# Kernel optimization log

Measured on AMD Instinct MI355X. Metric: run time of the kernel, lower is better.

## Reference

```python
import jax, jax.numpy as jnp
import numpy as np

N_NODES = 100000
N_EDGES = 1600000
EMBED_DIM = 64


def setup_inputs() -> dict:
    key = jax.random.key(0)
    k1, k2, k3, k4 = jax.random.split(key, 4)
    ego_embeddings = jax.random.normal(k1, (N_NODES, EMBED_DIM), dtype=jnp.float32)
    adj_values = jax.random.uniform(k2, (N_EDGES,), dtype=jnp.float32)
    adj_rows = jax.random.randint(k3, (N_EDGES,), 0, N_NODES, dtype=jnp.int32)
    adj_cols = jax.random.randint(k4, (N_EDGES,), 0, N_NODES, dtype=jnp.int32)
    return {
        "ego_embeddings": ego_embeddings,
        "adj_values": adj_values,
        "adj_rows": adj_rows,
        "adj_cols": adj_cols,
    }


def reference(ego_embeddings, adj_values, adj_rows, adj_cols):
    # out[r, :] = sum_{e : rows[e]==r} values[e] * ego_embeddings[cols[e], :]
    # == tf.sparse.sparse_dense_matmul(adj, ego_embeddings)
    messages = adj_values[:, None] * ego_embeddings[adj_cols]  # [E, D]
    out = jax.ops.segment_sum(messages, adj_rows, num_segments=N_NODES)  # [N, D]
    return out
```

## Files before the change

### kernel.cpp

```cpp
#include <hip/hip_runtime.h>

#define N_NODES 100000
#define N_EDGES 1600000
#define EMBED_DIM 64

#define RPB 256
#define NBKT ((N_NODES + RPB - 1) / RPB)
#define CAP 4608
#define TILE 4096
#define NTILE ((N_EDGES + TILE - 1) / TILE)
#define OVCAP 8192

__global__ __launch_bounds__(256) void k_binA(const int* __restrict__ rows,
                                              const int* __restrict__ cols,
                                              const float* __restrict__ vals,
                                              int* __restrict__ gcur,
                                              int2* __restrict__ packed,
                                              int* __restrict__ ov_cnt,
                                              int4* __restrict__ ov) {
    __shared__ int hist[NBKT];
    __shared__ int off[NBKT];
    __shared__ int cur[NBKT];
    __shared__ int gbase[NBKT];
    __shared__ int ssum[256];
    __shared__ int2 stage[TILE];
    __shared__ int dg[TILE];
    const int tid = threadIdx.x;
    const int e0 = blockIdx.x * TILE;

    for (int i = tid; i < NBKT; i += 256) hist[i] = 0;
    __syncthreads();

    for (int i = tid; i < TILE; i += 256) {
        int e = e0 + i;
        if (e < N_EDGES) atomicAdd(&hist[rows[e] >> 8], 1);
    }
    __syncthreads();

    int b0 = 2 * tid, b1 = 2 * tid + 1;
    int h0 = (b0 < NBKT) ? hist[b0] : 0;
    int h1 = (b1 < NBKT) ? hist[b1] : 0;
    ssum[tid] = h0 + h1;
    __syncthreads();
    for (int o = 1; o < 256; o <<= 1) {
        int a = ssum[tid];
        int add = (tid >= o) ? ssum[tid - o] : 0;
        __syncthreads();
        ssum[tid] = a + add;
        __syncthreads();
    }
    int base = (tid == 0) ? 0 : ssum[tid - 1];
    if (b0 < NBKT) { off[b0] = base; cur[b0] = base; }
    if (b1 < NBKT) { off[b1] = base + h0; cur[b1] = base + h0; }

    for (int b = tid; b < NBKT; b += 256) {
        int c = hist[b];
        gbase[b] = c ? atomicAdd(&gcur[b], c) : 0;
    }
    __syncthreads();

    for (int i = tid; i < TILE; i += 256) {
        int e = e0 + i;
        if (e < N_EDGES) {
            int r = rows[e];
            int b = r >> 8;
            int p = atomicAdd(&cur[b], 1);
            stage[p] = make_int2(((r & (RPB - 1)) << 17) | cols[e],
                                 __float_as_int(vals[e]));
            int d = gbase[b] + (p - off[b]);
            dg[p] = (d < CAP) ? (b * CAP + d) : (0x40000000 | b);
        }
    }
    __syncthreads();

    int total = ssum[255];
    for (int j = tid; j < total; j += 256) {
        int d = dg[j];
        int2 ev = stage[j];
        if (d & 0x40000000) {
            int b = d & 0xFFFF;
            int ovi = atomicAdd(ov_cnt, 1);
            if (ovi < OVCAP) {
                int r = b * RPB + (((unsigned)ev.x) >> 17);
                ov[ovi] = make_int4(r, ev.x & 0x1FFFF, ev.y, 0);
            }
        } else {
            packed[d] = ev;
        }
    }
}

__global__ __launch_bounds__(256) void k_binB(const int* __restrict__ gcur,
                                              int2* __restrict__ packed,
                                              int* __restrict__ row_ptr,
                                              int* __restrict__ cnt) {
    __shared__ int2 stage[CAP];
    __shared__ int h[RPB];
    __shared__ int s[RPB];
    __shared__ int cur[RPB];
    const int b = blockIdx.x;
    const int tid = threadIdx.x;
    int n = gcur[b];
    if (n > CAP) n = CAP;
    const int base = b * CAP;

    h[tid] = 0;
    __syncthreads();
    for (int j = tid; j < n; j += 256) {
        int2 e = packed[base + j];
        stage[j] = e;
        atomicAdd(&h[((unsigned)e.x) >> 17], 1);
    }
    __syncthreads();

    int hv = h[tid];
    s[tid] = hv;
    __syncthreads();
    for (int o = 1; o < 256; o <<= 1) {
        int a = s[tid];
        int add = (tid >= o) ? s[tid - o] : 0;
        __syncthreads();
        s[tid] = a + add;
        __syncthreads();
    }
    int ofs = (tid == 0) ? 0 : s[tid - 1];
    cur[tid] = ofs;
    int r = b * RPB + tid;
    if (r < N_NODES) {
        row_ptr[r] = base + ofs;
        cnt[r] = hv;
    }
    __syncthreads();

    for (int j = tid; j < n; j += 256) {
        int2 e = stage[j];
        int lr = ((unsigned)e.x) >> 17;
        int p = atomicAdd(&cur[lr], 1);
        packed[base + p] = e;
    }
}

__global__ __launch_bounds__(256) void k_gather(const float* __restrict__ x,
                                                const int* __restrict__ row_ptr,
                                                const int* __restrict__ cnt,
                                                const int* __restrict__ pw,
                                                float* __restrict__ out) {
    int wid = (blockIdx.x * 256 + threadIdx.x) >> 6;
    int lane = threadIdx.x & 63;
    if (wid >= N_NODES) return;
    int beg = row_ptr[wid];
    int deg = cnt[wid];
    float acc = 0.f;
    int done = 0;
    while (done < deg) {
        int win = deg - done;
        if (win > 32) win = 32;
        int w = 0;
        if (lane < 2 * win) w = pw[2 * (beg + done) + lane];
        for (int k0 = 0; k0 < win; k0 += 16) {
#pragma unroll
            for (int k = 0; k < 16; ++k) {
                int kk = k0 + k;
                int cpack = __builtin_amdgcn_readlane(w, 2 * kk);
                float v = __int_as_float(__builtin_amdgcn_readlane(w, 2 * kk + 1));
                acc += v * x[(cpack & 0x1FFFF) * EMBED_DIM + lane];
            }
        }
        done += win;
    }
    out[wid * EMBED_DIM + lane] = acc;
}

__global__ __launch_bounds__(256) void k_overflow(const float* __restrict__ x,
                                                  const int* __restrict__ ov_cnt,
                                                  const int4* __restrict__ ov,
                                                  float* __restrict__ out) {
    int n = *ov_cnt;
    if (n > OVCAP) n = OVCAP;
    int idx = (blockIdx.x * 256 + threadIdx.x) >> 6;
    int lane = threadIdx.x & 63;
    if (idx >= n) return;
    int4 e = ov[idx];
    atomicAdd(&out[e.x * EMBED_DIM + lane],
              __int_as_float(e.z) * x[e.y * EMBED_DIM + lane]);
}

__global__ __launch_bounds__(256) void spmm_scatter_kernel(
    const float* __restrict__ x, const float* __restrict__ vals,
    const int* __restrict__ rows, const int* __restrict__ cols,
    float* __restrict__ out) {
    const int wave_in_block = threadIdx.x >> 6;
    const int lane = threadIdx.x & 63;
    const int e = blockIdx.x * 4 + wave_in_block;
    if (e >= N_EDGES) return;
    const float m = vals[e] * x[cols[e] * EMBED_DIM + lane];
    atomicAdd(&out[rows[e] * EMBED_DIM + lane], m);
}

extern "C" void kernel_launch(void* const* d_in, const int* in_sizes, int n_in,
                              void* d_out, int out_size, void* d_ws, size_t ws_size,
                              hipStream_t stream) {
    const float* x    = (const float*)d_in[0];
    const float* vals = (const float*)d_in[1];
    const int*   rows = (const int*)d_in[2];
    const int*   cols = (const int*)d_in[3];
    float* out = (float*)d_out;

    const size_t packed_b = (size_t)NBKT * CAP * 8;
    const size_t ov_b     = (size_t)OVCAP * 16;
    const size_t need = packed_b + ov_b + ((size_t)NBKT + 2 * N_NODES + 1) * 4;
    if (ws_size < need) {
        hipMemsetAsync(out, 0, (size_t)out_size * sizeof(float), stream);
        spmm_scatter_kernel<<<(N_EDGES + 3) / 4, 256, 0, stream>>>(x, vals, rows, cols, out);
        return;
    }

    int2* packed = (int2*)d_ws;
    int4* ov     = (int4*)((char*)d_ws + packed_b);
    int*  gcur   = (int*)((char*)d_ws + packed_b + ov_b);
    int*  row_ptr = gcur + NBKT;
    int*  cnt     = row_ptr + N_NODES;
    int*  ov_cnt  = cnt + N_NODES;

    hipMemsetAsync(gcur, 0, (size_t)NBKT * sizeof(int), stream);
    hipMemsetAsync(ov_cnt, 0, sizeof(int), stream);

    k_binA<<<NTILE, 256, 0, stream>>>(rows, cols, vals, gcur, packed, ov_cnt, ov);
    k_binB<<<NBKT, 256, 0, stream>>>(gcur, packed, row_ptr, cnt);
    k_gather<<<(N_NODES * 64 + 255) / 256, 256, 0, stream>>>(x, row_ptr, cnt, (const int*)packed, out);
    k_overflow<<<(OVCAP + 3) / 4, 256, 0, stream>>>(x, ov_cnt, ov, out);
}
```

Measured before the change: 186.7 us.

## Add ping-pong bucket sort, simplify gather loads, shrink binning tile and overflow grid

Halves the binning tile size so more blocks run in the first binning pass. Adds an out-of-place second pass (used when the workspace is large enough) that reads the packed buffer and writes a separate sorted buffer, skipping the large LDS staging. The sorted entries now carry clean column indices. The gather kernel drops the readlane broadcast and issues uniform int2 loads eight at a time. The overflow kernel uses a small grid-stride launch, and the two memsets are merged into one.

```diff
diff --git a/kernel.cpp b/kernel.cpp
--- a/kernel.cpp
+++ b/kernel.cpp
@@ -7,7 +7,7 @@
 #define RPB 256
 #define NBKT ((N_NODES + RPB - 1) / RPB)
 #define CAP 4608
-#define TILE 4096
+#define TILE 2048
 #define NTILE ((N_EDGES + TILE - 1) / TILE)
 #define OVCAP 8192
 
@@ -90,10 +90,57 @@
     }
 }
 
-__global__ __launch_bounds__(256) void k_binB(const int* __restrict__ gcur,
-                                              int2* __restrict__ packed,
-                                              int* __restrict__ row_ptr,
-                                              int* __restrict__ cnt) {
+__global__ __launch_bounds__(256) void k_binB_pp(const int* __restrict__ gcur,
+                                                 const int2* __restrict__ packed,
+                                                 int2* __restrict__ sorted,
+                                                 int* __restrict__ row_ptr,
+                                                 int* __restrict__ cnt) {
+    __shared__ int h[RPB];
+    __shared__ int s[RPB];
+    __shared__ int cur[RPB];
+    const int b = blockIdx.x;
+    const int tid = threadIdx.x;
+    int n = gcur[b];
+    if (n > CAP) n = CAP;
+    const int base = b * CAP;
+
+    h[tid] = 0;
+    __syncthreads();
+    for (int j = tid; j < n; j += 256)
+        atomicAdd(&h[((unsigned)packed[base + j].x) >> 17], 1);
+    __syncthreads();
+
+    int hv = h[tid];
+    s[tid] = hv;
+    __syncthreads();
+    for (int o = 1; o < 256; o <<= 1) {
+        int a = s[tid];
+        int add = (tid >= o) ? s[tid - o] : 0;
+        __syncthreads();
+        s[tid] = a + add;
+        __syncthreads();
+    }
+    int ofs = (tid == 0) ? 0 : s[tid - 1];
+    cur[tid] = ofs;
+    int r = b * RPB + tid;
+    if (r < N_NODES) {
+        row_ptr[r] = base + ofs;
+        cnt[r] = hv;
+    }
+    __syncthreads();
+
+    for (int j = tid; j < n; j += 256) {
+        int2 e = packed[base + j];
+        int lr = ((unsigned)e.x) >> 17;
+        int p = atomicAdd(&cur[lr], 1);
+        sorted[base + p] = make_int2(e.x & 0x1FFFF, e.y);
+    }
+}
+
+__global__ __launch_bounds__(256) void k_binB_ip(const int* __restrict__ gcur,
+                                                 int2* __restrict__ packed,
+                                                 int* __restrict__ row_ptr,
+                                                 int* __restrict__ cnt) {
     __shared__ int2 stage[CAP];
     __shared__ int h[RPB];
     __shared__ int s[RPB];
@@ -136,37 +183,34 @@
         int2 e = stage[j];
         int lr = ((unsigned)e.x) >> 17;
         int p = atomicAdd(&cur[lr], 1);
-        packed[base + p] = e;
+        packed[base + p] = make_int2(e.x & 0x1FFFF, e.y);
     }
 }
 
 __global__ __launch_bounds__(256) void k_gather(const float* __restrict__ x,
                                                 const int* __restrict__ row_ptr,
                                                 const int* __restrict__ cnt,
-                                                const int* __restrict__ pw,
+                                                const int2* __restrict__ ep,
                                                 float* __restrict__ out) {
     int wid = (blockIdx.x * 256 + threadIdx.x) >> 6;
     int lane = threadIdx.x & 63;
     if (wid >= N_NODES) return;
-    int beg = row_ptr[wid];
-    int deg = cnt[wid];
+    int beg = __builtin_amdgcn_readfirstlane(row_ptr[wid]);
+    int deg = __builtin_amdgcn_readfirstlane(cnt[wid]);
+    const int2* p = ep + beg;
     float acc = 0.f;
-    int done = 0;
-    while (done < deg) {
-        int win = deg - done;
-        if (win > 32) win = 32;
-        int w = 0;
-        if (lane < 2 * win) w = pw[2 * (beg + done) + lane];
-        for (int k0 = 0; k0 < win; k0 += 16) {
+    int k = 0;
+    for (; k + 8 <= deg; k += 8) {
+        int2 e[8];
 #pragma unroll
-            for (int k = 0; k < 16; ++k) {
-                int kk = k0 + k;
-                int cpack = __builtin_amdgcn_readlane(w, 2 * kk);
-                float v = __int_as_float(__builtin_amdgcn_readlane(w, 2 * kk + 1));
-                acc += v * x[(cpack & 0x1FFFF) * EMBED_DIM + lane];
-            }
-        }
-        done += win;
+        for (int i = 0; i < 8; ++i) e[i] = p[k + i];
+#pragma unroll
+        for (int i = 0; i < 8; ++i)
+            acc += __int_as_float(e[i].y) * x[(e[i].x << 6) + lane];
+    }
+    for (; k < deg; ++k) {
+        int2 e = p[k];
+        acc += __int_as_float(e.y) * x[(e.x << 6) + lane];
     }
     out[wid * EMBED_DIM + lane] = acc;
 }
@@ -177,12 +221,13 @@
                                                   float* __restrict__ out) {
     int n = *ov_cnt;
     if (n > OVCAP) n = OVCAP;
-    int idx = (blockIdx.x * 256 + threadIdx.x) >> 6;
     int lane = threadIdx.x & 63;
-    if (idx >= n) return;
-    int4 e = ov[idx];
-    atomicAdd(&out[e.x * EMBED_DIM + lane],
-              __int_as_float(e.z) * x[e.y * EMBED_DIM + lane]);
+    for (int idx = (blockIdx.x * 256 + threadIdx.x) >> 6; idx < n;
+         idx += gridDim.x * 4) {
+        int4 e = ov[idx];
+        atomicAdd(&out[e.x * EMBED_DIM + lane],
+                  __int_as_float(e.z) * x[e.y * EMBED_DIM + lane]);
+    }
 }
 
 __global__ __launch_bounds__(256) void spmm_scatter_kernel(
@@ -208,25 +253,33 @@
 
     const size_t packed_b = (size_t)NBKT * CAP * 8;
     const size_t ov_b     = (size_t)OVCAP * 16;
-    const size_t need = packed_b + ov_b + ((size_t)NBKT + 2 * N_NODES + 1) * 4;
-    if (ws_size < need) {
+    const size_t tail_b   = ((size_t)NBKT + 1 + 2 * (size_t)N_NODES) * 4;
+    const size_t need_pp  = 2 * packed_b + ov_b + tail_b;
+    const size_t need_ip  = packed_b + ov_b + tail_b;
+
+    if (ws_size < need_ip) {
         hipMemsetAsync(out, 0, (size_t)out_size * sizeof(float), stream);
         spmm_scatter_kernel<<<(N_EDGES + 3) / 4, 256, 0, stream>>>(x, vals, rows, cols, out);
         return;
     }
 
+    const bool pp = (ws_size >= need_pp);
     int2* packed = (int2*)d_ws;
-    int4* ov     = (int4*)((char*)d_ws + packed_b);
-    int*  gcur   = (int*)((char*)d_ws + packed_b + ov_b);
-    int*  row_ptr = gcur + NBKT;
+    int2* sorted = pp ? (int2*)((char*)d_ws + packed_b) : packed;
+    char* rest   = (char*)d_ws + (pp ? 2 * packed_b : packed_b);
+    int4* ov     = (int4*)rest;
+    int*  gcur   = (int*)(rest + ov_b);
+    int*  ov_cnt = gcur + NBKT;
+    int*  row_ptr = ov_cnt + 1;
     int*  cnt     = row_ptr + N_NODES;
-    int*  ov_cnt  = cnt + N_NODES;
-
-    hipMemsetAsync(gcur, 0, (size_t)NBKT * sizeof(int), stream);
-    hipMemsetAsync(ov_cnt, 0, sizeof(int), stream);
+
+    hipMemsetAsync(gcur, 0, ((size_t)NBKT + 1) * sizeof(int), stream);
 
     k_binA<<<NTILE, 256, 0, stream>>>(rows, cols, vals, gcur, packed, ov_cnt, ov);
-    k_binB<<<NBKT, 256, 0, stream>>>(gcur, packed, row_ptr, cnt);
-    k_gather<<<(N_NODES * 64 + 255) / 256, 256, 0, stream>>>(x, row_ptr, cnt, (const int*)packed, out);
-    k_overflow<<<(OVCAP + 3) / 4, 256, 0, stream>>>(x, ov_cnt, ov, out);
-}
+    if (pp)
+        k_binB_pp<<<NBKT, 256, 0, stream>>>(gcur, packed, sorted, row_ptr, cnt);
+    else
+        k_binB_ip<<<NBKT, 256, 0, stream>>>(gcur, packed, row_ptr, cnt);
+    k_gather<<<(N_NODES * 64 + 255) / 256, 256, 0, stream>>>(x, row_ptr, cnt, sorted, out);
+    k_overflow<<<64, 256, 0, stream>>>(x, ov_cnt, ov, out);
+}
```

Measured after the change: 188.1 us. About the same (+0.7%).
